# Kernel tuning notes

Hardware: AMD Instinct MI355X
Metric: run time of the kernel (lower is better)

Reference implementation:

```python
import jax, jax.numpy as jnp
import numpy as np

N_CANDIDATE_K = 10
CENTER_RADIUS = 2.5
STRIDE = 32.0
ALPHA, GAMMA = 0.25, 2.0


def cxcywh_to_xyxy(b):
    cx, cy, w, h = b[..., 0], b[..., 1], b[..., 2], b[..., 3]
    return jnp.stack([cx - 0.5 * w, cy - 0.5 * h, cx + 0.5 * w, cy + 0.5 * h], axis=-1)


def box_iou_xyxy(a, b):
    # a: [Q,4], b: [G,4] -> iou [Q,G], union [Q,G]
    area_a = (a[:, 2] - a[:, 0]) * (a[:, 3] - a[:, 1])
    area_b = (b[:, 2] - b[:, 0]) * (b[:, 3] - b[:, 1])
    lt = jnp.maximum(a[:, None, :2], b[None, :, :2])
    rb = jnp.minimum(a[:, None, 2:], b[None, :, 2:])
    wh = jnp.clip(rb - lt, 0.0)
    inter = wh[..., 0] * wh[..., 1]
    union = area_a[:, None] + area_b[None, :] - inter
    return inter / union, union


def generalized_box_iou(a, b):
    iou, union = box_iou_xyxy(a, b)
    lt = jnp.minimum(a[:, None, :2], b[None, :, :2])
    rb = jnp.maximum(a[:, None, 2:], b[None, :, 2:])
    wh = jnp.clip(rb - lt, 0.0)
    enclose = wh[..., 0] * wh[..., 1]
    return iou - (enclose - union) / enclose


def in_boxes_info(boxes, gts):
    # boxes: [Q,4] cxcywh, gts: [G,4] cxcywh
    xy = cxcywh_to_xyxy(gts)  # [G,4]
    ax = boxes[:, 0:1]  # [Q,1]
    ay = boxes[:, 1:2]
    in_box = (ax > xy[:, 0]) & (ax < xy[:, 2]) & (ay > xy[:, 1]) & (ay < xy[:, 3])  # [Q,G]
    r = CENTER_RADIUS / STRIDE
    in_ctr = (ax > gts[:, 0] - r) & (ax < gts[:, 0] + r) & (ay > gts[:, 1] - r) & (ay < gts[:, 1] + r)
    fg_mask = in_box.any(axis=1) | in_ctr.any(axis=1)  # [Q]
    return fg_mask, in_box & in_ctr


def build_cost(prob, boxes, labels, gt_boxes):
    # prob [Q,C], boxes [Q,4], labels [G] int, gt_boxes [G,4] -> cost [Q,G], ious [Q,G]
    fg_mask, iibc = in_boxes_info(boxes, gt_boxes)
    bx = cxcywh_to_xyxy(boxes)
    gx = cxcywh_to_xyxy(gt_boxes)
    ious, _ = box_iou_xyxy(bx, gx)
    p = prob[:, labels]  # gather per-gt class prob -> [Q,G]
    neg = (1.0 - ALPHA) * p ** GAMMA * (-jnp.log1p(-(p - 1e-8) - 1.0 + 1.0) if False else -jnp.log(1.0 - p + 1e-8))
    pos = ALPHA * (1.0 - p) ** GAMMA * (-jnp.log(p + 1e-8))
    cost_class = pos - neg
    cost_giou = -generalized_box_iou(bx, gx)
    cost = cost_class + 3.0 * cost_giou + 100.0 * (1.0 - iibc.astype(cost_class.dtype))
    cost = cost + 10000.0 * (1.0 - fg_mask.astype(cost.dtype))[:, None]
    return cost, ious


def dynamic_k_matching(cost, ious):
    Q, G = cost.shape
    # dynamic k per gt from sum of top-10 ious (truncated to int, min 1)
    topk_ious, _ = jax.lax.top_k(ious.T, N_CANDIDATE_K)  # [G,10]
    dyn_k = jnp.maximum(topk_ious.sum(-1).astype(jnp.int32), 1)  # [G]
    # per-gt lowest-cost topk via rank matrix (rank of each query in ascending cost)
    ranks = jnp.argsort(jnp.argsort(cost, axis=0), axis=0)
    matching = (ranks < dyn_k[None, :]).astype(cost.dtype)  # [Q,G]
    # resolve anchors matched to >1 gt: keep only their argmin-cost gt
    anchor_matching_gt = matching.sum(axis=1)
    stale_mask = anchor_matching_gt > 1  # (reused stale inside while loop, as in torch source)
    row_argmin = jnp.argmin(cost, axis=1)
    onehot = jax.nn.one_hot(row_argmin, G, dtype=matching.dtype)
    matching = jnp.where(stale_mask[:, None], onehot, matching)
    qids = jnp.arange(Q)

    def cond(state):
        _, m = state
        return (m.sum(axis=0) == 0).any()

    def body(state):
        c, m = state
        pred = (m.sum(axis=0) == 0).any()  # gate for vmap safety
        matched_q = m.sum(axis=1) > 0
        c2 = c + 100000.0 * matched_q[:, None].astype(c.dtype)
        unmatched = m.sum(axis=0) == 0
        col_argmin = jnp.argmin(c2, axis=0)  # [G]
        add = (qids[:, None] == col_argmin[None, :]) & unmatched[None, :]
        m2 = jnp.where(add, jnp.asarray(1.0, c.dtype), m)
        fix = (m2.sum(axis=1) > 1).any()
        row_am = jnp.argmin(c2, axis=1)
        oh = jax.nn.one_hot(row_am, G, dtype=m2.dtype)
        m3 = jnp.where(fix & stale_mask[:, None], oh, m2)
        return (jnp.where(pred, c2, c), jnp.where(pred, m3, m))

    cost_f, matching = jax.lax.while_loop(cond, body, (cost, matching))
    selected_query = matching.sum(axis=1) > 0  # [Q] bool
    gt_assign = jnp.argmax(matching, axis=1).astype(jnp.int32)  # [Q], valid where selected
    masked_cost = jnp.where(matching > 0, cost_f, jnp.inf)
    matched_query_id = jnp.argmin(masked_cost, axis=0).astype(jnp.int32)  # [G]
    return selected_query, gt_assign, matched_query_id


def reference(pred_logits, pred_boxes, tgt_labels, tgt_boxes):
    prob = jax.nn.sigmoid(pred_logits)

    def per_image(p, b, l, g):
        cost, ious = build_cost(p, b, l, g)
        return dynamic_k_matching(cost, ious)

    return jax.vmap(per_image)(prob, pred_boxes, tgt_labels, tgt_boxes)


def setup_inputs() -> dict:
    key = jax.random.key(0)
    B, Q, C, G = 16, 8400, 80, 64
    k1, k2, k3, k4 = jax.random.split(key, 4)

    def make_boxes(kk, shape):
        ka, kb = jax.random.split(kk)
        cxcy = jax.random.uniform(ka, shape + (2,), minval=0.1, maxval=0.9, dtype=jnp.float32)
        wh = jax.random.uniform(kb, shape + (2,), minval=0.05, maxval=0.3, dtype=jnp.float32)
        return jnp.concatenate([cxcy, wh], axis=-1)

    return {
        "pred_logits": jax.random.normal(k1, (B, Q, C), dtype=jnp.float32),
        "pred_boxes": make_boxes(k2, (B, Q)),
        "tgt_labels": jax.random.randint(k3, (B, G), 0, C),
        "tgt_boxes": make_boxes(k4, (B, G)),
    }
```

## Files before the change

kernel.cpp:

```cpp
#include <hip/hip_runtime.h>
#include <cstdint>
#include <cstddef>


static constexpr int Bn = 16;
static constexpr int Qn = 8400;
static constexpr int Cn = 80;
static constexpr int Gn = 64;
#define TPB 512
#define MLIST_CAP 1536
#define STALE_CAP 320

__device__ __forceinline__ unsigned int ordf(float f) {
    unsigned int u = __float_as_uint(f);
    return u ^ ((unsigned int)((int)u >> 31) | 0x80000000u);
}
__device__ __forceinline__ float inv_ordf(unsigned int o) {
    unsigned int u = (o & 0x80000000u) ? (o ^ 0x80000000u) : ~o;
    return __uint_as_float(u);
}
__device__ __forceinline__ float replay_penalty(float v, unsigned int k) {
    for (unsigned int t = 0; t < k; ++t) v += 100000.0f;
    return v;
}

__global__ __launch_bounds__(256)
void build_cost_kernel(const float* __restrict__ logits,
                       const float* __restrict__ pboxes,
                       const int*   __restrict__ labels,
                       const float* __restrict__ gboxes,
                       float* __restrict__ cost_cm,
                       float* __restrict__ ious_cm,
                       unsigned char* __restrict__ rowarg)
{
    const int b = blockIdx.y;
    const int q = blockIdx.x * blockDim.x + threadIdx.x;

    __shared__ float gx0[Gn], gy0[Gn], gx1[Gn], gy1[Gn];
    __shared__ float gcx[Gn], gcy[Gn], gar[Gn];
    __shared__ int   glab[Gn];
    if (threadIdx.x < Gn) {
        int g = threadIdx.x;
        const float* gb = &gboxes[((size_t)b*Gn + g)*4];
        float cx = gb[0], cy = gb[1], w = gb[2], h = gb[3];
        float x0 = cx - 0.5f*w, y0 = cy - 0.5f*h;
        float x1 = cx + 0.5f*w, y1 = cy + 0.5f*h;
        gx0[g]=x0; gy0[g]=y0; gx1[g]=x1; gy1[g]=y1;
        gcx[g]=cx; gcy[g]=cy;
        gar[g]=(x1-x0)*(y1-y0);
        glab[g]=labels[(size_t)b*Gn + g];
    }
    __syncthreads();
    if (q >= Qn) return;

    const float* pb = &pboxes[((size_t)b*Qn + q)*4];
    float cx = pb[0], cy = pb[1], w = pb[2], h = pb[3];
    float ax0 = cx - 0.5f*w, ay0 = cy - 0.5f*h;
    float ax1 = cx + 0.5f*w, ay1 = cy + 0.5f*h;
    float areaA = (ax1-ax0)*(ay1-ay0);
    const float r = 2.5f/32.0f;

    bool anyBox=false, anyCtr=false;
    for (int g=0; g<Gn; ++g) {
        bool ib = (cx>gx0[g]) && (cx<gx1[g]) && (cy>gy0[g]) && (cy<gy1[g]);
        bool ic = (cx>gcx[g]-r) && (cx<gcx[g]+r) && (cy>gcy[g]-r) && (cy<gcy[g]+r);
        anyBox |= ib; anyCtr |= ic;
    }
    float fgterm = (anyBox || anyCtr) ? 0.0f : 10000.0f;

    const float* lrow = &logits[((size_t)b*Qn + q)*Cn];
    float rmin = __builtin_inff(); int rarg = 0;
    size_t obase = ((size_t)b*Gn)*Qn + q;
    for (int g=0; g<Gn; ++g) {
        float X0=gx0[g], Y0=gy0[g], X1=gx1[g], Y1=gy1[g];
        float ltx=fmaxf(ax0,X0), lty=fmaxf(ay0,Y0);
        float rbx=fminf(ax1,X1), rby=fminf(ay1,Y1);
        float wx=fmaxf(rbx-ltx,0.f), wy=fmaxf(rby-lty,0.f);
        float inter=wx*wy;
        float uni=(areaA+gar[g])-inter;
        float iou=inter/uni;
        float l2x=fminf(ax0,X0), l2y=fminf(ay0,Y0);
        float r2x=fmaxf(ax1,X1), r2y=fmaxf(ay1,Y1);
        float ex=fmaxf(r2x-l2x,0.f), ey=fmaxf(r2y-l2y,0.f);
        float enc=ex*ey;
        float giou = iou - (enc-uni)/enc;
        float xlg = lrow[glab[g]];
        float p = 1.0f/(1.0f+expf(-xlg));
        float neg = 0.75f*(p*p)*(-logf(1.0f-p+1e-8f));
        float pos = 0.25f*((1.0f-p)*(1.0f-p))*(-logf(p+1e-8f));
        float cls = pos - neg;
        bool ib = (cx>X0)&&(cx<X1)&&(cy>Y0)&&(cy<Y1);
        bool ic = (cx>gcx[g]-r)&&(cx<gcx[g]+r)&&(cy>gcy[g]-r)&&(cy<gcy[g]+r);
        float iibc = (ib&&ic) ? 1.0f : 0.0f;
        float cost = ((cls + 3.0f*(-giou)) + 100.0f*(1.0f-iibc)) + fgterm;
        cost_cm[obase + (size_t)g*Qn] = cost;
        ious_cm[obase + (size_t)g*Qn] = iou;
        if (cost < rmin) { rmin = cost; rarg = g; }
    }
    rowarg[(size_t)b*Qn + q] = (unsigned char)rarg;
}

__device__ __forceinline__ void hist_find(unsigned int* hist, unsigned int* chunk,
                                          unsigned int* s_bin, unsigned int* s_cb,
                                          unsigned int want, int tid)
{
    if (tid < 64) {
        unsigned int s = 0;
        for (int i = 0; i < 64; ++i) s += hist[tid*64 + i];
        chunk[tid] = s;
    }
    __syncthreads();
    if (tid == 0) {
        unsigned int acc = 0; int c = 0;
        for (; c < 63; ++c) { if (acc + chunk[c] >= want) break; acc += chunk[c]; }
        int bbase = c*64; unsigned int bb = 0;
        for (; bb < 63; ++bb) { unsigned int h = hist[bbase+bb]; if (acc + h >= want) break; acc += h; }
        *s_bin = (unsigned int)(bbase + bb);
        *s_cb  = acc;
    }
    __syncthreads();
}

__global__ __launch_bounds__(256)
void column_select_kernel(const float* __restrict__ cost_all,
                          const float* __restrict__ ious_all,
                          int*   __restrict__ dynk_all,
                          float* __restrict__ poolv_all,
                          int*   __restrict__ poolq_all)
{
    const int g = blockIdx.x, b = blockIdx.y, tid = threadIdx.x;
    const float* ccol = cost_all + ((size_t)b*Gn + g)*Qn;
    const float* icol = ious_all + ((size_t)b*Gn + g)*Qn;

    __shared__ unsigned int hist[4096];
    __shared__ unsigned int chunk[64];
    __shared__ unsigned int s_bin1, s_bin2, s_bin3, s_cb1, s_cb2, s_cb3;
    __shared__ unsigned int s_nb, s_nt;
    __shared__ float pv[64]; __shared__ int pq[64];
    __shared__ float sv[64]; __shared__ int sq[64];
    __shared__ int tq[64];
    __shared__ float tl[256][10];

    {
        float tv[10];
        #pragma unroll
        for (int i=0;i<10;i++) tv[i] = -1.0f;
        for (int j=tid; j<Qn; j+=256) {
            float v = icol[j];
            if (v > tv[9]) {
                int k = 9;
                #pragma unroll
                for (int s=9; s>0; --s) { if (v > tv[s-1]) { tv[s]=tv[s-1]; k=s-1; } }
                tv[k]=v;
            }
        }
        #pragma unroll
        for (int i=0;i<10;i++) tl[tid][i]=tv[i];
        __syncthreads();
        for (int s=128; s>0; s>>=1) {
            if (tid < s) {
                float a[10], c[10];
                #pragma unroll
                for (int i=0;i<10;i++){ a[i]=tl[tid][i]; c[i]=tl[tid+s][i]; }
                float m[10]; int ia=0, ic=0;
                #pragma unroll
                for (int i=0;i<10;i++) {
                    float va = a[ia], vc = c[ic];
                    if (va >= vc) { m[i]=va; ++ia; } else { m[i]=vc; ++ic; }
                }
                #pragma unroll
                for (int i=0;i<10;i++) tl[tid][i]=m[i];
            }
            __syncthreads();
        }
        if (tid == 0) {
            float s = 0.0f;
            #pragma unroll
            for (int i=0;i<10;i++) s += tl[0][i];
            int k = (int)s;
            if (k < 1) k = 1;
            if (k > 10) k = 10;
            dynk_all[b*Gn + g] = k;
        }
    }
    __syncthreads();

    {
        const unsigned int want = 64;
        for (int i=tid;i<4096;i+=256) hist[i]=0u;
        __syncthreads();
        for (int j=tid;j<Qn;j+=256) { unsigned int od=ordf(ccol[j]); atomicAdd(&hist[od>>20],1u); }
        __syncthreads();
        hist_find(hist, chunk, &s_bin1, &s_cb1, want, tid);
        for (int i=tid;i<4096;i+=256) hist[i]=0u;
        __syncthreads();
        for (int j=tid;j<Qn;j+=256) {
            unsigned int od=ordf(ccol[j]);
            if ((od>>20)==s_bin1) atomicAdd(&hist[(od>>8)&0xFFFu],1u);
        }
        __syncthreads();
        hist_find(hist, chunk, &s_bin2, &s_cb2, want - s_cb1, tid);
        for (int i=tid;i<4096;i+=256) hist[i]=0u;
        __syncthreads();
        unsigned int hi24 = (s_bin1<<12) | s_bin2;
        for (int j=tid;j<Qn;j+=256) {
            unsigned int od=ordf(ccol[j]);
            if ((od>>8)==hi24) atomicAdd(&hist[od&0xFFu],1u);
        }
        __syncthreads();
        hist_find(hist, chunk, &s_bin3, &s_cb3, want - s_cb1 - s_cb2, tid);

        const unsigned int thr = (s_bin1<<20) | (s_bin2<<8) | s_bin3;
        const unsigned int c_strict = s_cb1 + s_cb2 + s_cb3;
        const unsigned int t_take = want - c_strict;
        if (tid==0) { s_nb=0u; s_nt=0u; }
        __syncthreads();
        for (int j=tid;j<Qn;j+=256) {
            float v = ccol[j];
            unsigned int od = ordf(v);
            if (od < thr) {
                unsigned int pos = atomicAdd(&s_nb,1u);
                if (pos < 64u) { pv[pos]=v; pq[pos]=j; }
            } else if (od == thr) {
                unsigned int pos = atomicAdd(&s_nt,1u);
                if (pos < 64u) tq[pos]=j;
            }
        }
        __syncthreads();
        if (tid==0) {
            float thrv = inv_ordf(thr);
            int nt = (int)s_nt; if (nt > 64) nt = 64;
            for (int i=1;i<nt;++i){ int x=tq[i]; int k=i; while(k>0 && tq[k-1]>x){tq[k]=tq[k-1];--k;} tq[k]=x; }
            for (unsigned int r=0; r<t_take && (int)r<nt; ++r) { pv[c_strict+r]=thrv; pq[c_strict+r]=tq[r]; }
        }
        __syncthreads();
        if (tid < 64) {
            float v = pv[tid]; int qq = pq[tid];
            int rank = 0;
            for (int j=0;j<64;++j) {
                float u = pv[j]; int uq = pq[j];
                if (u < v || (u==v && uq<qq)) ++rank;
            }
            sv[rank]=v; sq[rank]=qq;
        }
        __syncthreads();
        if (tid < 64) {
            size_t base = ((size_t)b*Gn + g)*64 + tid;
            poolv_all[base] = sv[tid];
            poolq_all[base] = sq[tid];
        }
    }
}

__global__ __launch_bounds__(TPB)
void match_kernel(const float* __restrict__ cost_all,
                  const unsigned char* __restrict__ rowarg_all,
                  const int*   __restrict__ dynk_all,
                  const float* __restrict__ poolv_all,
                  const int*   __restrict__ poolq_all,
                  unsigned long long* __restrict__ mmask_all,
                  int* __restrict__ out)
{
    const int b = blockIdx.x;
    const int tid = threadIdx.x;
    const float* costb = cost_all + (size_t)b*Gn*Qn;
    const unsigned char* rarg = rowarg_all + (size_t)b*Qn;
    unsigned long long* mmask = mmask_all + (size_t)b*Qn;

    __shared__ __align__(16) unsigned long long s_pool_raw[2048];
    __shared__ int s_pq[Gn*64];
    __shared__ unsigned short s_kcnt[Qn];
    __shared__ int s_mlist[MLIST_CAP];
    __shared__ int s_staleq[STALE_CAP], s_stalec[STALE_CAP];
    __shared__ float s_mv[TPB]; __shared__ int s_mi[TPB];
    __shared__ int s_dynk[Gn];
    __shared__ unsigned int s_colcnt[Gn];
    __shared__ int s_winq[Gn];
    __shared__ unsigned long long s_unm, s_fbmask;
    __shared__ int s_mn, s_scnt, s_fix;

    float* s_pv = (float*)s_pool_raw;

    for (int q=tid; q<Qn; q+=TPB) s_kcnt[q]=0;
    for (int i=tid; i<Gn*64; i+=TPB) {
        size_t base = (size_t)b*Gn*64 + i;
        s_pv[i] = poolv_all[base];
        s_pq[i] = poolq_all[base];
    }
    if (tid < Gn) { s_dynk[tid] = dynk_all[b*Gn+tid]; s_colcnt[tid]=0u; }
    for (int q=tid; q<Qn; q+=TPB) mmask[q]=0ull;
    if (tid==0) { s_mn=0; s_scnt=0; s_fix=0; }
    __syncthreads();

    if (tid < Gn) {
        int k = s_dynk[tid];
        unsigned long long bit = 1ull<<tid;
        for (int t=0; t<k; ++t) {
            int q = s_pq[tid*64 + t];
            unsigned long long old = atomicOr(&mmask[q], bit);
            if (old == 0ull) {
                int pos = atomicAdd(&s_mn,1);
                if (pos < MLIST_CAP) s_mlist[pos]=q;
            }
        }
    }
    __syncthreads();
    int mn = s_mn; if (mn > MLIST_CAP) mn = MLIST_CAP;

    for (int j=tid; j<mn; j+=TPB) {
        int q = s_mlist[j];
        unsigned long long m = atomicOr(&mmask[q], 0ull);
        if (__popcll(m) > 1) {
            int pos = atomicAdd(&s_scnt,1);
            int rp = rarg[q];
            if (pos < STALE_CAP) { s_staleq[pos]=q; s_stalec[pos]=rp; }
            atomicExch(&mmask[q], 1ull<<rp);
        }
    }
    __syncthreads();
    const int scnt = (s_scnt < STALE_CAP) ? s_scnt : STALE_CAP;
    for (int j=tid; j<mn; j+=TPB) {
        unsigned long long m = atomicOr(&mmask[s_mlist[j]], 0ull);
        while (m) { int gg = __ffsll(m)-1; m &= m-1ull; atomicAdd(&s_colcnt[gg],1u); }
    }
    __syncthreads();

    for (int iter=0; iter<1024; ++iter) {
        if (tid < 64) {
            unsigned long long bal = __ballot(s_colcnt[tid]==0u);
            if (tid==0) { s_unm = bal; s_fbmask = 0ull; }
        }
        __syncthreads();
        const unsigned long long unm = s_unm;
        if (unm == 0ull) break;
        mn = s_mn; if (mn > MLIST_CAP) mn = MLIST_CAP;

        for (int j=tid; j<mn; j+=TPB) s_kcnt[s_mlist[j]]++;
        __syncthreads();

        int wq = -1;
        if (tid < 64 && ((unm>>tid)&1ull)) {
            for (int t=0; t<64; ++t) {
                int q = s_pq[tid*64 + t];
                if (s_kcnt[q]==0) { wq=q; break; }
            }
            if (wq < 0) atomicOr(&s_fbmask, 1ull<<tid);
        }
        __syncthreads();
        unsigned long long fb = s_fbmask;
        while (fb) {
            int c = __ffsll(fb)-1; fb &= fb-1ull;
            float bv=__builtin_inff(); int bq=0x7fffffff;
            for (int j=tid; j<Qn; j+=TPB) {
                if (s_kcnt[j]==0) {
                    float v = costb[(size_t)c*Qn + j];
                    if (v<bv || (v==bv && j<bq)) { bv=v; bq=j; }
                }
            }
            s_mv[tid]=bv; s_mi[tid]=bq;
            __syncthreads();
            for (int s=TPB/2; s>0; s>>=1) {
                if (tid<s) {
                    float v2=s_mv[tid+s]; int q2=s_mi[tid+s];
                    if (v2<s_mv[tid] || (v2==s_mv[tid] && q2<s_mi[tid])) { s_mv[tid]=v2; s_mi[tid]=q2; }
                }
                __syncthreads();
            }
            if (tid==0) s_winq[c]=s_mi[0];
            __syncthreads();
        }
        if (tid<64 && wq<0 && ((unm>>tid)&1ull)) wq = s_winq[tid];

        if (tid<64 && ((unm>>tid)&1ull) && wq>=0 && wq<Qn) {
            unsigned long long bit = 1ull<<tid;
            unsigned long long old = atomicOr(&mmask[wq], bit);
            if (old==0ull) {
                int pos = atomicAdd(&s_mn,1);
                if (pos < MLIST_CAP) s_mlist[pos]=wq;
            }
            if (__popcll(old|bit) > 1) s_fix = 1;
            atomicAdd(&s_colcnt[tid],1u);
        }
        __syncthreads();

        if (s_fix) {
            for (int j=tid; j<scnt; j+=TPB) {
                int q = s_staleq[j];
                unsigned int kk = s_kcnt[q];
                float best=__builtin_inff(); int bg=0;
                for (int gg=0; gg<Gn; ++gg) {
                    float v = replay_penalty(costb[(size_t)gg*Qn + q], kk);
                    if (v < best) { best=v; bg=gg; }
                }
                int oc = s_stalec[j];
                if (bg != oc) {
                    atomicAdd(&s_colcnt[oc], (unsigned int)-1);
                    atomicAdd(&s_colcnt[bg], 1u);
                    s_stalec[j] = bg;
                    atomicExch(&mmask[q], 1ull<<bg);
                }
            }
        }
        __syncthreads();
    }

    __syncthreads();
    mn = s_mn; if (mn > MLIST_CAP) mn = MLIST_CAP;
    unsigned long long* s_mcache = s_pool_raw;
    for (int j=tid; j<mn; j+=TPB) s_mcache[j] = atomicOr(&mmask[s_mlist[j]], 0ull);
    for (int q=tid; q<Qn; q+=TPB) {
        out[(size_t)b*Qn + q] = 0;
        out[(size_t)Bn*Qn + (size_t)b*Qn + q] = 0;
    }
    __syncthreads();
    for (int j=tid; j<mn; j+=TPB) {
        int q = s_mlist[j];
        unsigned long long m = s_mcache[j];
        out[(size_t)b*Qn + q] = 1;
        out[(size_t)Bn*Qn + (size_t)b*Qn + q] = __ffsll(m)-1;
    }
    __syncthreads();
    {
        const int g = tid>>3, p = tid&7;
        float best=__builtin_inff(); int bq=0x7fffffff;
        for (int j=p; j<mn; j+=8) {
            unsigned long long m = s_mcache[j];
            if ((m>>g)&1ull) {
                int q = s_mlist[j];
                float v = replay_penalty(costb[(size_t)g*Qn+q], s_kcnt[q]);
                if (v<best || (v==best && q<bq)) { best=v; bq=q; }
            }
        }
        s_mv[tid]=best; s_mi[tid]=bq;
    }
    __syncthreads();
    if (tid < Gn) {
        float best=__builtin_inff(); int bq=0x7fffffff;
        #pragma unroll
        for (int u=0;u<8;++u) {
            float v=s_mv[tid*8+u]; int qq=s_mi[tid*8+u];
            if (v<best || (v==best && qq<bq)) { best=v; bq=qq; }
        }
        if (bq>=Qn) bq=0;
        out[(size_t)2*Bn*Qn + (size_t)b*Gn + tid] = bq;
    }
}

extern "C" void kernel_launch(void* const* d_in, const int* in_sizes, int n_in,
                              void* d_out, int out_size, void* d_ws, size_t ws_size,
                              hipStream_t stream)
{
    const float* logits = (const float*)d_in[0];
    const float* pboxes = (const float*)d_in[1];
    const int*   labels = (const int*)d_in[2];
    const float* gboxes = (const float*)d_in[3];
    int* out = (int*)d_out;

    char* ws = (char*)d_ws;
    size_t off = 0;
    float* cost_cm = (float*)(ws + off); off += (size_t)Bn*Gn*Qn*sizeof(float);
    float* ious_cm = (float*)(ws + off); off += (size_t)Bn*Gn*Qn*sizeof(float);
    unsigned long long* mmask = (unsigned long long*)(ws + off); off += (size_t)Bn*Qn*sizeof(unsigned long long);
    float* poolv = (float*)(ws + off); off += (size_t)Bn*Gn*64*sizeof(float);
    int*   poolq = (int*)(ws + off);   off += (size_t)Bn*Gn*64*sizeof(int);
    int*   dynk  = (int*)(ws + off);   off += (size_t)Bn*Gn*sizeof(int);
    unsigned char* rowarg = (unsigned char*)(ws + off); off += (size_t)Bn*Qn;

    dim3 g1((Qn+255)/256, Bn);
    build_cost_kernel<<<g1, 256, 0, stream>>>(logits, pboxes, labels, gboxes,
                                              cost_cm, ious_cm, rowarg);
    dim3 g2(Gn, Bn);
    column_select_kernel<<<g2, 256, 0, stream>>>(cost_cm, ious_cm, dynk, poolv, poolq);
    match_kernel<<<Bn, TPB, 0, stream>>>(cost_cm, rowarg, dynk, poolv, poolq, mmask, out);
}
```

Measured before the change: 294.9 us.

## Stage logits tile in LDS and cache ordered cost column in shared memory

The build_cost kernel now loads each block's 128 logit rows into padded shared memory with coalesced float4 loads, so the per-gt label gathers are served from LDS instead of strided global reads. The column_select kernel moves to 512 threads and keeps the 8400 ordered-key cost values of its column in shared memory, so the later radix-select passes and the final collection pass no longer reload from global memory. This raises LDS use per block to about 50KB, which may lower occupancy. The top-10 IoU merge tree now runs over 512 partial lists instead of 256.

```diff
diff --git a/kernel.cpp b/kernel.cpp
--- a/kernel.cpp
+++ b/kernel.cpp
@@ -10,6 +10,7 @@
 #define TPB 512
 #define MLIST_CAP 1536
 #define STALE_CAP 320
+#define QT 128
 
 __device__ __forceinline__ unsigned int ordf(float f) {
     unsigned int u = __float_as_uint(f);
@@ -24,7 +25,7 @@
     return v;
 }
 
-__global__ __launch_bounds__(256)
+__global__ __launch_bounds__(QT)
 void build_cost_kernel(const float* __restrict__ logits,
                        const float* __restrict__ pboxes,
                        const int*   __restrict__ labels,
@@ -34,13 +35,18 @@
                        unsigned char* __restrict__ rowarg)
 {
     const int b = blockIdx.y;
-    const int q = blockIdx.x * blockDim.x + threadIdx.x;
-
+    const int q0 = blockIdx.x * QT;
+    const int tid = threadIdx.x;
+    const int q = q0 + tid;
+    const int qmax = (Qn - q0 < QT) ? (Qn - q0) : QT;
+
+    __shared__ float sl[QT*81];
     __shared__ float gx0[Gn], gy0[Gn], gx1[Gn], gy1[Gn];
     __shared__ float gcx[Gn], gcy[Gn], gar[Gn];
     __shared__ int   glab[Gn];
-    if (threadIdx.x < Gn) {
-        int g = threadIdx.x;
+
+    if (tid < Gn) {
+        int g = tid;
         const float* gb = &gboxes[((size_t)b*Gn + g)*4];
         float cx = gb[0], cy = gb[1], w = gb[2], h = gb[3];
         float x0 = cx - 0.5f*w, y0 = cy - 0.5f*h;
@@ -50,8 +56,16 @@
         gar[g]=(x1-x0)*(y1-y0);
         glab[g]=labels[(size_t)b*Gn + g];
     }
-    __syncthreads();
-    if (q >= Qn) return;
+    for (int i = tid; i < QT*20; i += QT) {
+        int row = i / 20, c4 = i % 20;
+        if (row < qmax) {
+            const float4 v = *(const float4*)&logits[((size_t)b*Qn + q0 + row)*Cn + c4*4];
+            float* d = &sl[row*81 + c4*4];
+            d[0]=v.x; d[1]=v.y; d[2]=v.z; d[3]=v.w;
+        }
+    }
+    __syncthreads();
+    if (tid >= qmax) return;
 
     const float* pb = &pboxes[((size_t)b*Qn + q)*4];
     float cx = pb[0], cy = pb[1], w = pb[2], h = pb[3];
@@ -68,9 +82,9 @@
     }
     float fgterm = (anyBox || anyCtr) ? 0.0f : 10000.0f;
 
-    const float* lrow = &logits[((size_t)b*Qn + q)*Cn];
     float rmin = __builtin_inff(); int rarg = 0;
     size_t obase = ((size_t)b*Gn)*Qn + q;
+    const float* myrow = &sl[tid*81];
     for (int g=0; g<Gn; ++g) {
         float X0=gx0[g], Y0=gy0[g], X1=gx1[g], Y1=gy1[g];
         float ltx=fmaxf(ax0,X0), lty=fmaxf(ay0,Y0);
@@ -84,7 +98,7 @@
         float ex=fmaxf(r2x-l2x,0.f), ey=fmaxf(r2y-l2y,0.f);
         float enc=ex*ey;
         float giou = iou - (enc-uni)/enc;
-        float xlg = lrow[glab[g]];
+        float xlg = myrow[glab[g]];
         float p = 1.0f/(1.0f+expf(-xlg));
         float neg = 0.75f*(p*p)*(-logf(1.0f-p+1e-8f));
         float pos = 0.25f*((1.0f-p)*(1.0f-p))*(-logf(p+1e-8f));
@@ -121,7 +135,7 @@
     __syncthreads();
 }
 
-__global__ __launch_bounds__(256)
+__global__ __launch_bounds__(512)
 void column_select_kernel(const float* __restrict__ cost_all,
                           const float* __restrict__ ious_all,
                           int*   __restrict__ dynk_all,
@@ -132,20 +146,20 @@
     const float* ccol = cost_all + ((size_t)b*Gn + g)*Qn;
     const float* icol = ious_all + ((size_t)b*Gn + g)*Qn;
 
-    __shared__ unsigned int hist[4096];
+    __shared__ __align__(16) char u_smem[50048];
     __shared__ unsigned int chunk[64];
     __shared__ unsigned int s_bin1, s_bin2, s_bin3, s_cb1, s_cb2, s_cb3;
     __shared__ unsigned int s_nb, s_nt;
     __shared__ float pv[64]; __shared__ int pq[64];
     __shared__ float sv[64]; __shared__ int sq[64];
     __shared__ int tq[64];
-    __shared__ float tl[256][10];
 
     {
+        float (*tl)[10] = (float(*)[10])u_smem;
         float tv[10];
         #pragma unroll
         for (int i=0;i<10;i++) tv[i] = -1.0f;
-        for (int j=tid; j<Qn; j+=256) {
+        for (int j=tid; j<Qn; j+=512) {
             float v = icol[j];
             if (v > tv[9]) {
                 int k = 9;
@@ -157,7 +171,7 @@
         #pragma unroll
         for (int i=0;i<10;i++) tl[tid][i]=tv[i];
         __syncthreads();
-        for (int s=128; s>0; s>>=1) {
+        for (int s=256; s>0; s>>=1) {
             if (tid < s) {
                 float a[10], c[10];
                 #pragma unroll
@@ -186,25 +200,34 @@
     __syncthreads();
 
     {
+        unsigned int* s_ord = (unsigned int*)u_smem;
+        unsigned int* hist  = (unsigned int*)(u_smem + 33664);
         const unsigned int want = 64;
-        for (int i=tid;i<4096;i+=256) hist[i]=0u;
-        __syncthreads();
-        for (int j=tid;j<Qn;j+=256) { unsigned int od=ordf(ccol[j]); atomicAdd(&hist[od>>20],1u); }
+
+        for (int i=tid;i<4096;i+=512) hist[i]=0u;
+        __syncthreads();
+        for (int j=tid;j<Qn;j+=512) {
+            unsigned int od = ordf(ccol[j]);
+            s_ord[j] = od;
+            atomicAdd(&hist[od>>20],1u);
+        }
         __syncthreads();
         hist_find(hist, chunk, &s_bin1, &s_cb1, want, tid);
-        for (int i=tid;i<4096;i+=256) hist[i]=0u;
-        __syncthreads();
-        for (int j=tid;j<Qn;j+=256) {
-            unsigned int od=ordf(ccol[j]);
+
+        for (int i=tid;i<4096;i+=512) hist[i]=0u;
+        __syncthreads();
+        for (int j=tid;j<Qn;j+=512) {
+            unsigned int od = s_ord[j];
             if ((od>>20)==s_bin1) atomicAdd(&hist[(od>>8)&0xFFFu],1u);
         }
         __syncthreads();
         hist_find(hist, chunk, &s_bin2, &s_cb2, want - s_cb1, tid);
-        for (int i=tid;i<4096;i+=256) hist[i]=0u;
+
+        for (int i=tid;i<4096;i+=512) hist[i]=0u;
         __syncthreads();
         unsigned int hi24 = (s_bin1<<12) | s_bin2;
-        for (int j=tid;j<Qn;j+=256) {
-            unsigned int od=ordf(ccol[j]);
+        for (int j=tid;j<Qn;j+=512) {
+            unsigned int od = s_ord[j];
             if ((od>>8)==hi24) atomicAdd(&hist[od&0xFFu],1u);
         }
         __syncthreads();
@@ -215,12 +238,11 @@
         const unsigned int t_take = want - c_strict;
         if (tid==0) { s_nb=0u; s_nt=0u; }
         __syncthreads();
-        for (int j=tid;j<Qn;j+=256) {
-            float v = ccol[j];
-            unsigned int od = ordf(v);
+        for (int j=tid;j<Qn;j+=512) {
+            unsigned int od = s_ord[j];
             if (od < thr) {
                 unsigned int pos = atomicAdd(&s_nb,1u);
-                if (pos < 64u) { pv[pos]=v; pq[pos]=j; }
+                if (pos < 64u) { pv[pos]=inv_ordf(od); pq[pos]=j; }
             } else if (od == thr) {
                 unsigned int pos = atomicAdd(&s_nt,1u);
                 if (pos < 64u) tq[pos]=j;
@@ -466,10 +488,10 @@
     int*   dynk  = (int*)(ws + off);   off += (size_t)Bn*Gn*sizeof(int);
     unsigned char* rowarg = (unsigned char*)(ws + off); off += (size_t)Bn*Qn;
 
-    dim3 g1((Qn+255)/256, Bn);
-    build_cost_kernel<<<g1, 256, 0, stream>>>(logits, pboxes, labels, gboxes,
-                                              cost_cm, ious_cm, rowarg);
+    dim3 g1((Qn + QT - 1)/QT, Bn);
+    build_cost_kernel<<<g1, QT, 0, stream>>>(logits, pboxes, labels, gboxes,
+                                             cost_cm, ious_cm, rowarg);
     dim3 g2(Gn, Bn);
-    column_select_kernel<<<g2, 256, 0, stream>>>(cost_cm, ious_cm, dynk, poolv, poolq);
+    column_select_kernel<<<g2, 512, 0, stream>>>(cost_cm, ious_cm, dynk, poolv, poolq);
     match_kernel<<<Bn, TPB, 0, stream>>>(cost_cm, rowarg, dynk, poolv, poolq, mmask, out);
 }
```

After: 323.2 us. +9.6%, slower.
